# Optimization experiments

Hardware: AMD Instinct MI355X
Metric: run time of the kernel (lower is better)

Reference implementation:

```python
import math
import jax, jax.numpy as jnp
import numpy as np

B, T, D, NH = 4, 2048, 1024, 16
HS = D // NH
N_BUCKETS = 32
MAX_DIST = 128


def _relative_position_bucket(rp):
    # bidirectional T5 bucketing, n_buckets=32, max_distance=128
    nb = N_BUCKETS // 2  # 16
    buckets = (rp > 0).astype(jnp.int32) * nb
    rp = jnp.abs(rp)
    max_exact = nb // 2  # 8
    is_small = rp < max_exact
    me = max_exact - 1   # 7
    nbm = nb - 1         # 15
    rp_safe = jnp.maximum(rp, 1).astype(jnp.float32)
    rp_large = me + (jnp.log(rp_safe / me) / math.log(MAX_DIST / me) * (nbm - me)).astype(jnp.int32)
    rp_large = jnp.minimum(rp_large, nbm)
    buckets = buckets + jnp.where(is_small, rp, rp_large)
    return buckets


def compute_bias(rel_emb, qT, kT):
    ctx = jnp.arange(qT, dtype=jnp.int32)[:, None]
    mem = jnp.arange(kT, dtype=jnp.int32)[None, :]
    bucket = _relative_position_bucket(mem - ctx)  # [qT, kT]
    values = rel_emb[bucket]                        # [qT, kT, NH]
    return jnp.transpose(values, (2, 0, 1))[None]   # [1, NH, qT, kT]


def setup_inputs() -> dict:
    key = jax.random.key(0)
    ks = jax.random.split(key, 6)
    s = 0.02
    return {
        "queries": jax.random.normal(ks[0], (B, T, D), jnp.float32),
        "Wq": jax.random.normal(ks[1], (D, D), jnp.float32) * s,
        "Wk": jax.random.normal(ks[2], (D, D), jnp.float32) * s,
        "Wv": jax.random.normal(ks[3], (D, D), jnp.float32) * s,
        "Wo": jax.random.normal(ks[4], (D, D), jnp.float32) * s,
        "rel_emb": jax.random.normal(ks[5], (N_BUCKETS, NH), jnp.float32) * s,
    }


def reference(queries, Wq, Wk, Wv, Wo, rel_emb):
    b, t, d = queries.shape
    def split_heads(x):
        return jnp.transpose(x.reshape(b, t, NH, HS), (0, 2, 1, 3))  # [B, nh, T, hs]
    q = split_heads(queries @ Wq.T)
    k = split_heads(queries @ Wk.T)
    v = split_heads(queries @ Wv.T)
    att = jnp.einsum('bhqd,bhkd->bhqk', q, k) * (1.0 / math.sqrt(HS))
    att = att + compute_bias(rel_emb, t, t)
    att = jax.nn.softmax(att, axis=-1)
    o = jnp.einsum('bhqk,bhkd->bhqd', att, v)
    o = jnp.transpose(o, (0, 2, 1, 3)).reshape(b, t, d)
    return o @ Wo.T
```

## Files before the change

### kernel.cpp

```cpp
#include <hip/hip_runtime.h>
#include <math.h>

#define T_SEQ 2048
#define D_MODEL 1024
#define NHEADS 16
#define HSZ 64
#define BATCH 4

typedef __bf16 bf16x8 __attribute__((ext_vector_type(8)));
typedef __bf16 bf16x4 __attribute__((ext_vector_type(4)));
typedef short short4v __attribute__((ext_vector_type(4)));
typedef float f32x4 __attribute__((ext_vector_type(4)));
typedef float f32x16 __attribute__((ext_vector_type(16)));

__device__ __forceinline__ unsigned short f2bf(float f) {
    unsigned int u = __builtin_bit_cast(unsigned int, f);
    u += 0x7fff + ((u >> 16) & 1);
    return (unsigned short)(u >> 16);
}

__device__ __forceinline__ unsigned int pk2bf(float a, float b) {
#if __has_builtin(__builtin_amdgcn_cvt_pk_bf16_f32)
    typedef __bf16 bf16x2_t __attribute__((ext_vector_type(2)));
    bf16x2_t v = __builtin_amdgcn_cvt_pk_bf16_f32(a, b);
    return __builtin_bit_cast(unsigned int, v);
#else
    return (unsigned int)f2bf(a) | ((unsigned int)f2bf(b) << 16);
#endif
}

__device__ __forceinline__ float fexp2(float x) {
#if __has_builtin(__builtin_amdgcn_exp2f)
    return __builtin_amdgcn_exp2f(x);
#else
    return __builtin_exp2f(x);
#endif
}

__device__ __forceinline__ void pl32swap(unsigned int& a, unsigned int& b) {
#if __has_builtin(__builtin_amdgcn_permlane32_swap)
    auto r = __builtin_amdgcn_permlane32_swap((int)a, (int)b, false, false);
    a = (unsigned int)r[0];
    b = (unsigned int)r[1];
#else
    unsigned int sa = (unsigned int)__shfl_xor((int)a, 32);
    unsigned int sb = (unsigned int)__shfl_xor((int)b, 32);
    const int hi = (int)((threadIdx.x & 63) >> 5);
    unsigned int na = hi ? sb : a;
    unsigned int nb = hi ? b : sa;
    a = na; b = nb;
#endif
}

__device__ __forceinline__ void gld_lds16(const void* g, void* lds) {
    __builtin_amdgcn_global_load_lds(
        (const __attribute__((address_space(1))) unsigned int*)g,
        (__attribute__((address_space(3))) unsigned int*)lds, 16, 0, 0);
}

__device__ __forceinline__ bf16x8 ld8(const unsigned short* p) {
    return *(const bf16x8*)p;
}

__device__ __forceinline__ float t5_bias(int delta, int h, const float* __restrict__ rel) {
    int bucket = delta > 0 ? 16 : 0;
    int arp = delta < 0 ? -delta : delta;
    if (arp < 8) {
        bucket += arp;
    } else {
        float f = logf((float)arp / 7.0f) * (8.0f / logf(128.0f / 7.0f));
        int rl = 7 + (int)f;
        bucket += rl < 15 ? rl : 15;
    }
    return rel[bucket * NHEADS + h] * 1.4426950408889634f;
}

__global__ void prep(const float* __restrict__ x,
                     const float* __restrict__ w0, const float* __restrict__ w1,
                     const float* __restrict__ w2, const float* __restrict__ w3,
                     unsigned short* __restrict__ Xbf,
                     unsigned short* __restrict__ Wbf) {
    int bid = blockIdx.x;
    int tid = threadIdx.x;
    if (bid < 8192) {
        int i = bid * 256 + tid;
        float4 v = ((const float4*)x)[i];
        ushort4 o;
        o.x = f2bf(v.x); o.y = f2bf(v.y); o.z = f2bf(v.z); o.w = f2bf(v.w);
        ((ushort4*)Xbf)[i] = o;
    } else {
        int wsel = (bid - 8192) >> 10;
        const float* srcs[4] = {w0, w1, w2, w3};
        int i = ((bid - 8192) & 1023) * 256 + tid;
        float4 v = ((const float4*)srcs[wsel])[i];
        ushort4 o;
        o.x = f2bf(v.x); o.y = f2bf(v.y); o.z = f2bf(v.z); o.w = f2bf(v.w);
        ((ushort4*)(Wbf + (size_t)wsel * 1048576))[i] = o;
    }
}

template<int MODE>
__global__ __launch_bounds__(256, 2) void gemm_bt(
    const unsigned short* __restrict__ A,
    const unsigned short* __restrict__ Bw,
    void* __restrict__ out)
{
    constexpr int K = 1024;
    __shared__ __align__(16) char smem[65536];

    const int tid  = threadIdx.x;
    const int wave = tid >> 6;
    const int lane = tid & 63;
    const int quad = lane >> 4;
    const int l16  = lane & 15;
    const int wm   = wave >> 1;
    const int wn   = wave & 1;

    constexpr int NWGX = (MODE == 4) ? 24 : 8;
    const int orig = blockIdx.x + blockIdx.y * NWGX;
    constexpr int CPX = (NWGX * 64) / 8;
    const int swz  = (orig & 7) * CPX + (orig >> 3);
    const int bn   = swz % NWGX;
    const int bm   = swz / NWGX;

    const int r_in = lane >> 3;
    const int lc   = (lane & 7) ^ r_in;

    f32x4 acc[4][4];
    #pragma unroll
    for (int m = 0; m < 4; ++m)
        #pragma unroll
        for (int n = 0; n < 4; ++n)
            acc[m][n] = f32x4{0.f, 0.f, 0.f, 0.f};

    const long a_row0 = (long)bm * 128;
    const long b_row0 = (long)bn * 128;

    {
        const int k0 = lc * 8;
        unsigned short* As_ = (unsigned short*)smem;
        unsigned short* Bs_ = (unsigned short*)(smem + 16384);
        #pragma unroll
        for (int c = 0; c < 4; ++c) {
            int cc = wave * 4 + c;
            int r  = cc * 8 + r_in;
            gld_lds16(A  + (a_row0 + r) * K + k0, &As_[cc * 512]);
            gld_lds16(Bw + (b_row0 + r) * K + k0, &Bs_[cc * 512]);
        }
    }

    for (int kt = 0; kt < K / 64; ++kt) {
        const int cur = kt & 1;
        __syncthreads();

        if (kt + 1 < K / 64) {
            const int k0 = (kt + 1) * 64 + lc * 8;
            unsigned short* As_ = (unsigned short*)(smem + (cur ^ 1) * 32768);
            unsigned short* Bs_ = (unsigned short*)(smem + (cur ^ 1) * 32768 + 16384);
            #pragma unroll
            for (int c = 0; c < 4; ++c) {
                int cc = wave * 4 + c;
                int r  = cc * 8 + r_in;
                gld_lds16(A  + (a_row0 + r) * K + k0, &As_[cc * 512]);
                gld_lds16(Bw + (b_row0 + r) * K + k0, &Bs_[cc * 512]);
            }
        }

        unsigned short* As = (unsigned short*)(smem + cur * 32768);
        unsigned short* Bs = (unsigned short*)(smem + cur * 32768 + 16384);

        bf16x8 af[4][2], bf[4][2];
        #pragma unroll
        for (int m = 0; m < 4; ++m)
            #pragma unroll
            for (int ks = 0; ks < 2; ++ks) {
                int r  = wm * 64 + m * 16 + l16;
                int pc = (ks * 4 + quad) ^ (r & 7);
                af[m][ks] = ld8(&As[r * 64 + pc * 8]);
            }
        #pragma unroll
        for (int n = 0; n < 4; ++n)
            #pragma unroll
            for (int ks = 0; ks < 2; ++ks) {
                int r  = wn * 64 + n * 16 + l16;
                int pc = (ks * 4 + quad) ^ (r & 7);
                bf[n][ks] = ld8(&Bs[r * 64 + pc * 8]);
            }
        #pragma unroll
        for (int ks = 0; ks < 2; ++ks)
            #pragma unroll
            for (int m = 0; m < 4; ++m)
                #pragma unroll
                for (int n = 0; n < 4; ++n)
                    acc[m][n] = __builtin_amdgcn_mfma_f32_16x16x32_bf16(
                        af[m][ks], bf[n][ks], acc[m][n], 0, 0, 0);
    }

    const int which = (MODE == 4) ? (bn >> 3) : 0;
    if (MODE == 3) {
        float* O = (float*)out;
        #pragma unroll
        for (int m = 0; m < 4; ++m) {
            int row = bm * 128 + wm * 64 + m * 16 + quad * 4;
            #pragma unroll
            for (int n = 0; n < 4; ++n) {
                int col = bn * 128 + wn * 64 + n * 16 + l16;
                #pragma unroll
                for (int r = 0; r < 4; ++r)
                    O[(long)(row + r) * 1024 + col] = acc[m][n][r];
            }
        }
    } else if (which == 2) {
        unsigned short* O = (unsigned short*)out + (size_t)2 * 8388608;
        #pragma unroll
        for (int m = 0; m < 4; ++m) {
            int row = bm * 128 + wm * 64 + m * 16 + quad * 4;
            int b = row >> 11, t = row & 2047;
            #pragma unroll
            for (int n = 0; n < 4; ++n) {
                int cl = (bn * 128 + wn * 64 + n * 16 + l16) & 1023;
                int h = cl >> 6, hs = cl & 63;
                ushort4 pk;
                pk.x = f2bf(acc[m][n][0]); pk.y = f2bf(acc[m][n][1]);
                pk.z = f2bf(acc[m][n][2]); pk.w = f2bf(acc[m][n][3]);
                *(ushort4*)&O[(long)((b * 16 + h) * 64 + hs) * 2048 + t] = pk;
            }
        }
    } else {
        __syncthreads();
        unsigned short* Ew = (unsigned short*)smem + wave * 4608;
        const float qs = (which == 0) ? 0.125f * 1.4426950408889634f : 1.0f;
        #pragma unroll
        for (int m = 0; m < 4; ++m)
            #pragma unroll
            for (int n = 0; n < 4; ++n)
                #pragma unroll
                for (int r = 0; r < 4; ++r)
                    Ew[(m * 16 + quad * 4 + r) * 72 + n * 16 + l16] =
                        f2bf(acc[m][n][r] * qs);
        asm volatile("s_waitcnt lgkmcnt(0)" ::: "memory");

        const int cl0 = (bn * 128 + wn * 64) & 1023;
        const int h   = cl0 >> 6;
        const int gr0 = bm * 128 + wm * 64;
        const int b   = gr0 >> 11, t0 = gr0 & 2047;
        unsigned short* O = (unsigned short*)out + (size_t)which * 8388608
                          + ((size_t)(b * 16 + h) * 2048 + t0) * 64;
        #pragma unroll
        for (int rr = 0; rr < 8; ++rr) {
            int row   = rr * 8 + (lane >> 3);
            int chunk = lane & 7;
            uint4 v = *(const uint4*)&Ew[row * 72 + chunk * 8];
            *(uint4*)&O[(size_t)row * 64 + chunk * 8] = v;
        }
    }
}

__global__ __launch_bounds__(256, 4) void attn(
    const unsigned short* __restrict__ Q,
    const unsigned short* __restrict__ Kb,
    const unsigned short* __restrict__ Vt,
    const float* __restrict__ rel,
    unsigned short* __restrict__ AO)
{
    __shared__ __align__(16) char smem[33824];
    unsigned short* KsB = (unsigned short*)smem;
    unsigned short* VsB = (unsigned short*)(smem + 16384);
    float*          Bb  = (float*)(smem + 32768);

    const int tid  = threadIdx.x;
    const int wave = tid >> 6;
    const int lane = tid & 63;
    const int l31  = lane & 31;
    const int h5   = lane >> 5;

    const int bh = blockIdx.y;
    const int b  = bh >> 4, h = bh & 15;
    const int q0 = blockIdx.x * 128;

    const unsigned short* Qg = Q  + (long)bh * T_SEQ * HSZ;
    const unsigned short* Kg = Kb + (long)bh * T_SEQ * HSZ;
    const unsigned short* Vg = Vt + (long)bh * HSZ * T_SEQ;

    const int r_in = lane >> 3;
    const int lc   = (lane & 7) ^ r_in;

    {
        #pragma unroll
        for (int c = 0; c < 2; ++c) {
            int cc = wave * 2 + c;
            int r  = cc * 8 + r_in;
            gld_lds16(Kg + (long)r * 64 + lc * 8, &KsB[cc * 512]);
            gld_lds16(Vg + (long)r * T_SEQ + lc * 8, &VsB[cc * 512]);
        }
    }

    for (int i = tid; i < 263; i += 256)
        Bb[i] = t5_bias(i - 131, h, rel);

    const int qrow_lane = q0 + wave * 32 + l31;
    bf16x8 qf[4];
    #pragma unroll
    for (int hsc = 0; hsc < 4; ++hsc)
        qf[hsc] = ld8(&Qg[(long)qrow_lane * 64 + hsc * 16 + h5 * 8]);

    f32x16 o0 = {0.f,0.f,0.f,0.f,0.f,0.f,0.f,0.f,0.f,0.f,0.f,0.f,0.f,0.f,0.f,0.f};
    f32x16 o1 = o0;
    float li = 0.0f;

    const float cneg = rel[15 * NHEADS + h] * 1.4426950408889634f;
    const float cpos = rel[31 * NHEADS + h] * 1.4426950408889634f;

    for (int kt = 0; kt < T_SEQ / 64; ++kt) {
        const int cur = kt & 1;
        __syncthreads();

        if (kt + 1 < T_SEQ / 64) {
            unsigned short* Kn = KsB + (cur ^ 1) * 4096;
            unsigned short* Vn = VsB + (cur ^ 1) * 4096;
            #pragma unroll
            for (int c = 0; c < 2; ++c) {
                int cc = wave * 2 + c;
                int r  = cc * 8 + r_in;
                gld_lds16(Kg + (long)((kt + 1) * 64 + r) * 64 + lc * 8, &Kn[cc * 512]);
                gld_lds16(Vg + (long)r * T_SEQ + (kt + 1) * 64 + lc * 8, &Vn[cc * 512]);
            }
        }

        const unsigned short* Ks = KsB + cur * 4096;
        const unsigned short* Vs = VsB + cur * 4096;

        const int lo = kt * 64 - q0 - 127;
        const int hi = kt * 64 + 63 - q0;
        const bool outband = (lo >= 128) || (hi <= -128);
        const float cb = (lo >= 128) ? cpos : cneg;

        #pragma unroll
        for (int tt = 0; tt < 2; ++tt) {
            const int rk = tt * 32 + l31;
            bf16x8 af[4];
            #pragma unroll
            for (int hsc = 0; hsc < 4; ++hsc)
                af[hsc] = ld8(&Ks[rk * 64 + (((hsc << 1) | h5) ^ (rk & 7)) * 8]);

            f32x16 s;
            if (outband) {
                #pragma unroll
                for (int e = 0; e < 16; ++e) s[e] = cb;
            } else {
                const int ibase = kt * 64 + tt * 32 + h5 * 4 + 131 - qrow_lane;
                #pragma unroll
                for (int g = 0; g < 4; ++g) {
                    int i0 = ibase + g * 8;
                    i0 = i0 < 0 ? 0 : (i0 > 259 ? 259 : i0);
                    #pragma unroll
                    for (int r = 0; r < 4; ++r) s[g * 4 + r] = Bb[i0 + r];
                }
            }

            __builtin_amdgcn_s_setprio(1);
            #pragma unroll
            for (int hsc = 0; hsc < 4; ++hsc)
                s = __builtin_amdgcn_mfma_f32_32x32x16_bf16(af[hsc], qf[hsc], s, 0, 0, 0);
            __builtin_amdgcn_s_setprio(0);

            float p[16];
            #pragma unroll
            for (int e = 0; e < 16; ++e) p[e] = fexp2(s[e]);
            {
                float t0 = (p[0]  + p[1])  + (p[2]  + p[3]);
                float t1 = (p[4]  + p[5])  + (p[6]  + p[7]);
                float t2 = (p[8]  + p[9])  + (p[10] + p[11]);
                float t3 = (p[12] + p[13]) + (p[14] + p[15]);
                li += (t0 + t1) + (t2 + t3);
            }

            unsigned int x0 = pk2bf(p[0],  p[1]),  x1 = pk2bf(p[2],  p[3]);
            unsigned int y0 = pk2bf(p[4],  p[5]),  y1 = pk2bf(p[6],  p[7]);
            unsigned int z0 = pk2bf(p[8],  p[9]),  z1 = pk2bf(p[10], p[11]);
            unsigned int u0 = pk2bf(p[12], p[13]), u1 = pk2bf(p[14], p[15]);
            pl32swap(x0, y0); pl32swap(x1, y1);
            pl32swap(z0, u0); pl32swap(z1, u1);
            uint4 pw0 = {x0, x1, y0, y1};
            uint4 pw1 = {z0, z1, u0, u1};
            bf16x8 pf[2] = {__builtin_bit_cast(bf16x8, pw0),
                            __builtin_bit_cast(bf16x8, pw1)};

            #pragma unroll
            for (int c = 0; c < 2; ++c) {
                const int tc = tt * 2 + c;
                const int rv0 = l31;
                const int rv1 = 32 + l31;
                bf16x8 vf0 = ld8(&Vs[rv0 * 64 + (((tc << 1) | h5) ^ (rv0 & 7)) * 8]);
                bf16x8 vf1 = ld8(&Vs[rv1 * 64 + (((tc << 1) | h5) ^ (rv1 & 7)) * 8]);
                __builtin_amdgcn_s_setprio(1);
                o0 = __builtin_amdgcn_mfma_f32_32x32x16_bf16(pf[c], vf0, o0, 0, 0, 0);
                o1 = __builtin_amdgcn_mfma_f32_32x32x16_bf16(pf[c], vf1, o1, 0, 0, 0);
                __builtin_amdgcn_s_setprio(0);
            }
        }
    }

    li += __shfl_xor(li, 32);
    const float inv = 1.0f / li;

    #pragma unroll
    for (int g = 0; g < 4; ++g) {
        #pragma unroll
        for (int r = 0; r < 4; ++r) {
            const int ql = g * 8 + h5 * 4 + r;
            const float iv = __shfl(inv, ql);
            const int qrow = q0 + wave * 32 + ql;
            unsigned short* dst =
                &AO[(long)(b * T_SEQ + qrow) * D_MODEL + h * 64 + l31];
            dst[0]  = f2bf(o0[g * 4 + r] * iv);
            dst[32] = f2bf(o1[g * 4 + r] * iv);
        }
    }
}

extern "C" void kernel_launch(void* const* d_in, const int* in_sizes, int n_in,
                              void* d_out, int out_size, void* d_ws, size_t ws_size,
                              hipStream_t stream) {
    const float* x   = (const float*)d_in[0];
    const float* wq  = (const float*)d_in[1];
    const float* wk  = (const float*)d_in[2];
    const float* wv  = (const float*)d_in[3];
    const float* wo  = (const float*)d_in[4];
    const float* rel = (const float*)d_in[5];

    char* ws = (char*)d_ws;
    unsigned short* Xbf = (unsigned short*)(ws);
    unsigned short* Wbf = (unsigned short*)(ws + (16l << 20));
    unsigned short* Qb  = (unsigned short*)(ws + (24l << 20));

    prep<<<12288, 256, 0, stream>>>(x, wq, wk, wv, wo, Xbf, Wbf);

    gemm_bt<4><<<dim3(24, 64), 256, 0, stream>>>(Xbf, Wbf, Qb);

    unsigned short* Kbf = Qb + 8388608;
    unsigned short* Vtb = Qb + 16777216;
    unsigned short* AO  = Xbf;
    attn<<<dim3(16, 64), 256, 0, stream>>>(Qb, Kbf, Vtb, rel, AO);

    gemm_bt<3><<<dim3(8, 64), 256, 0, stream>>>(AO, Wbf + 3 * 1048576, d_out);
}
```

Baseline: 272.3 us.

## Process two query tiles per attention block with 128-key tiles for K/V reuse

Each attention block now handles 256 query rows (two 128-row tiles per wave set) and streams 128-key K/V tiles, so every K/V tile loaded to LDS feeds twice as many MFMAs. This halves the grid, doubles LDS and roughly doubles per-thread accumulators, and the launch bound drops to 2 blocks per CU. The aim is to cut global/LDS K/V traffic and sync overhead per FLOP, at the cost of occupancy and fewer blocks (512) to spread over the CUs.

```diff
diff --git a/kernel.cpp b/kernel.cpp
--- a/kernel.cpp
+++ b/kernel.cpp
@@ -256,17 +256,17 @@
     }
 }
 
-__global__ __launch_bounds__(256, 4) void attn(
+__global__ __launch_bounds__(256, 2) void attn(
     const unsigned short* __restrict__ Q,
     const unsigned short* __restrict__ Kb,
     const unsigned short* __restrict__ Vt,
     const float* __restrict__ rel,
     unsigned short* __restrict__ AO)
 {
-    __shared__ __align__(16) char smem[33824];
+    __shared__ __align__(16) char smem[66592];
     unsigned short* KsB = (unsigned short*)smem;
-    unsigned short* VsB = (unsigned short*)(smem + 16384);
-    float*          Bb  = (float*)(smem + 32768);
+    unsigned short* VsB = (unsigned short*)(smem + 32768);
+    float*          Bb  = (float*)(smem + 65536);
 
     const int tid  = threadIdx.x;
     const int wave = tid >> 6;
@@ -276,7 +276,7 @@
 
     const int bh = blockIdx.y;
     const int b  = bh >> 4, h = bh & 15;
-    const int q0 = blockIdx.x * 128;
+    const int q0 = blockIdx.x * 256;
 
     const unsigned short* Qg = Q  + (long)bh * T_SEQ * HSZ;
     const unsigned short* Kg = Kb + (long)bh * T_SEQ * HSZ;
@@ -284,137 +284,165 @@
 
     const int r_in = lane >> 3;
     const int lc   = (lane & 7) ^ r_in;
+    const int vr_l = lane >> 4;
 
     {
         #pragma unroll
-        for (int c = 0; c < 2; ++c) {
-            int cc = wave * 2 + c;
-            int r  = cc * 8 + r_in;
-            gld_lds16(Kg + (long)r * 64 + lc * 8, &KsB[cc * 512]);
-            gld_lds16(Vg + (long)r * T_SEQ + lc * 8, &VsB[cc * 512]);
+        for (int c = 0; c < 4; ++c) {
+            int cc = wave * 4 + c;
+            int kr = cc * 8 + r_in;
+            gld_lds16(Kg + (long)kr * 64 + lc * 8, &KsB[cc * 512]);
+            int vr = cc * 4 + vr_l;
+            int vch = (lane & 15) ^ (vr & 7);
+            gld_lds16(Vg + (long)vr * T_SEQ + vch * 8, &VsB[cc * 512]);
         }
     }
 
     for (int i = tid; i < 263; i += 256)
         Bb[i] = t5_bias(i - 131, h, rel);
 
-    const int qrow_lane = q0 + wave * 32 + l31;
-    bf16x8 qf[4];
+    bf16x8 qf[2][4];
     #pragma unroll
-    for (int hsc = 0; hsc < 4; ++hsc)
-        qf[hsc] = ld8(&Qg[(long)qrow_lane * 64 + hsc * 16 + h5 * 8]);
-
-    f32x16 o0 = {0.f,0.f,0.f,0.f,0.f,0.f,0.f,0.f,0.f,0.f,0.f,0.f,0.f,0.f,0.f,0.f};
-    f32x16 o1 = o0;
-    float li = 0.0f;
+    for (int qt = 0; qt < 2; ++qt) {
+        const int qrow = q0 + qt * 128 + wave * 32 + l31;
+        #pragma unroll
+        for (int hsc = 0; hsc < 4; ++hsc)
+            qf[qt][hsc] = ld8(&Qg[(long)qrow * 64 + hsc * 16 + h5 * 8]);
+    }
+
+    f32x16 o[2][2];
+    float li[2] = {0.f, 0.f};
+    #pragma unroll
+    for (int qt = 0; qt < 2; ++qt)
+        #pragma unroll
+        for (int hst = 0; hst < 2; ++hst)
+            o[qt][hst] = f32x16{0.f,0.f,0.f,0.f,0.f,0.f,0.f,0.f,
+                                0.f,0.f,0.f,0.f,0.f,0.f,0.f,0.f};
 
     const float cneg = rel[15 * NHEADS + h] * 1.4426950408889634f;
     const float cpos = rel[31 * NHEADS + h] * 1.4426950408889634f;
 
-    for (int kt = 0; kt < T_SEQ / 64; ++kt) {
+    for (int kt = 0; kt < T_SEQ / 128; ++kt) {
         const int cur = kt & 1;
         __syncthreads();
 
-        if (kt + 1 < T_SEQ / 64) {
-            unsigned short* Kn = KsB + (cur ^ 1) * 4096;
-            unsigned short* Vn = VsB + (cur ^ 1) * 4096;
-            #pragma unroll
-            for (int c = 0; c < 2; ++c) {
-                int cc = wave * 2 + c;
-                int r  = cc * 8 + r_in;
-                gld_lds16(Kg + (long)((kt + 1) * 64 + r) * 64 + lc * 8, &Kn[cc * 512]);
-                gld_lds16(Vg + (long)r * T_SEQ + (kt + 1) * 64 + lc * 8, &Vn[cc * 512]);
-            }
-        }
-
-        const unsigned short* Ks = KsB + cur * 4096;
-        const unsigned short* Vs = VsB + cur * 4096;
-
-        const int lo = kt * 64 - q0 - 127;
-        const int hi = kt * 64 + 63 - q0;
-        const bool outband = (lo >= 128) || (hi <= -128);
-        const float cb = (lo >= 128) ? cpos : cneg;
-
-        #pragma unroll
-        for (int tt = 0; tt < 2; ++tt) {
+        if (kt + 1 < T_SEQ / 128) {
+            unsigned short* Kn = KsB + (cur ^ 1) * 8192;
+            unsigned short* Vn = VsB + (cur ^ 1) * 8192;
+            #pragma unroll
+            for (int c = 0; c < 4; ++c) {
+                int cc = wave * 4 + c;
+                int kr = cc * 8 + r_in;
+                gld_lds16(Kg + (long)((kt + 1) * 128 + kr) * 64 + lc * 8, &Kn[cc * 512]);
+                int vr = cc * 4 + vr_l;
+                int vch = (lane & 15) ^ (vr & 7);
+                gld_lds16(Vg + (long)vr * T_SEQ + (kt + 1) * 128 + vch * 8, &Vn[cc * 512]);
+            }
+        }
+
+        const unsigned short* Ks = KsB + cur * 8192;
+        const unsigned short* Vs = VsB + cur * 8192;
+
+        #pragma unroll
+        for (int tt = 0; tt < 4; ++tt) {
+            const int tok_lo = kt * 128 + tt * 32;
+
             const int rk = tt * 32 + l31;
             bf16x8 af[4];
             #pragma unroll
             for (int hsc = 0; hsc < 4; ++hsc)
                 af[hsc] = ld8(&Ks[rk * 64 + (((hsc << 1) | h5) ^ (rk & 7)) * 8]);
 
-            f32x16 s;
-            if (outband) {
-                #pragma unroll
-                for (int e = 0; e < 16; ++e) s[e] = cb;
-            } else {
-                const int ibase = kt * 64 + tt * 32 + h5 * 4 + 131 - qrow_lane;
-                #pragma unroll
-                for (int g = 0; g < 4; ++g) {
-                    int i0 = ibase + g * 8;
-                    i0 = i0 < 0 ? 0 : (i0 > 259 ? 259 : i0);
+            bf16x8 pf[2][2];
+            #pragma unroll
+            for (int qt = 0; qt < 2; ++qt) {
+                const int qlo = q0 + qt * 128 + wave * 32;
+                const int dmin = tok_lo - qlo - 31;
+                const int dmax = tok_lo + 31 - qlo;
+                f32x16 s;
+                if (dmin >= 128 || dmax <= -128) {
+                    const float cb = (dmin >= 128) ? cpos : cneg;
                     #pragma unroll
-                    for (int r = 0; r < 4; ++r) s[g * 4 + r] = Bb[i0 + r];
+                    for (int e = 0; e < 16; ++e) s[e] = cb;
+                } else {
+                    const int ibase = tok_lo + h5 * 4 + 131 - (qlo + l31);
+                    #pragma unroll
+                    for (int g = 0; g < 4; ++g) {
+                        int i0 = ibase + g * 8;
+                        i0 = i0 < 0 ? 0 : (i0 > 259 ? 259 : i0);
+                        #pragma unroll
+                        for (int r = 0; r < 4; ++r) s[g * 4 + r] = Bb[i0 + r];
+                    }
                 }
-            }
-
-            __builtin_amdgcn_s_setprio(1);
-            #pragma unroll
-            for (int hsc = 0; hsc < 4; ++hsc)
-                s = __builtin_amdgcn_mfma_f32_32x32x16_bf16(af[hsc], qf[hsc], s, 0, 0, 0);
-            __builtin_amdgcn_s_setprio(0);
-
-            float p[16];
-            #pragma unroll
-            for (int e = 0; e < 16; ++e) p[e] = fexp2(s[e]);
-            {
-                float t0 = (p[0]  + p[1])  + (p[2]  + p[3]);
-                float t1 = (p[4]  + p[5])  + (p[6]  + p[7]);
-                float t2 = (p[8]  + p[9])  + (p[10] + p[11]);
-                float t3 = (p[12] + p[13]) + (p[14] + p[15]);
-                li += (t0 + t1) + (t2 + t3);
-            }
-
-            unsigned int x0 = pk2bf(p[0],  p[1]),  x1 = pk2bf(p[2],  p[3]);
-            unsigned int y0 = pk2bf(p[4],  p[5]),  y1 = pk2bf(p[6],  p[7]);
-            unsigned int z0 = pk2bf(p[8],  p[9]),  z1 = pk2bf(p[10], p[11]);
-            unsigned int u0 = pk2bf(p[12], p[13]), u1 = pk2bf(p[14], p[15]);
-            pl32swap(x0, y0); pl32swap(x1, y1);
-            pl32swap(z0, u0); pl32swap(z1, u1);
-            uint4 pw0 = {x0, x1, y0, y1};
-            uint4 pw1 = {z0, z1, u0, u1};
-            bf16x8 pf[2] = {__builtin_bit_cast(bf16x8, pw0),
-                            __builtin_bit_cast(bf16x8, pw1)};
+
+                __builtin_amdgcn_s_setprio(1);
+                #pragma unroll
+                for (int hsc = 0; hsc < 4; ++hsc)
+                    s = __builtin_amdgcn_mfma_f32_32x32x16_bf16(af[hsc], qf[qt][hsc],
+                                                                s, 0, 0, 0);
+                __builtin_amdgcn_s_setprio(0);
+
+                float p[16];
+                #pragma unroll
+                for (int e = 0; e < 16; ++e) p[e] = fexp2(s[e]);
+                {
+                    float t0 = (p[0]  + p[1])  + (p[2]  + p[3]);
+                    float t1 = (p[4]  + p[5])  + (p[6]  + p[7]);
+                    float t2 = (p[8]  + p[9])  + (p[10] + p[11]);
+                    float t3 = (p[12] + p[13]) + (p[14] + p[15]);
+                    li[qt] += (t0 + t1) + (t2 + t3);
+                }
+
+                unsigned int x0 = pk2bf(p[0],  p[1]),  x1 = pk2bf(p[2],  p[3]);
+                unsigned int y0 = pk2bf(p[4],  p[5]),  y1 = pk2bf(p[6],  p[7]);
+                unsigned int z0 = pk2bf(p[8],  p[9]),  z1 = pk2bf(p[10], p[11]);
+                unsigned int u0 = pk2bf(p[12], p[13]), u1 = pk2bf(p[14], p[15]);
+                pl32swap(x0, y0); pl32swap(x1, y1);
+                pl32swap(z0, u0); pl32swap(z1, u1);
+                uint4 pw0 = {x0, x1, y0, y1};
+                uint4 pw1 = {z0, z1, u0, u1};
+                pf[qt][0] = __builtin_bit_cast(bf16x8, pw0);
+                pf[qt][1] = __builtin_bit_cast(bf16x8, pw1);
+            }
 
             #pragma unroll
             for (int c = 0; c < 2; ++c) {
-                const int tc = tt * 2 + c;
-                const int rv0 = l31;
-                const int rv1 = 32 + l31;
-                bf16x8 vf0 = ld8(&Vs[rv0 * 64 + (((tc << 1) | h5) ^ (rv0 & 7)) * 8]);
-                bf16x8 vf1 = ld8(&Vs[rv1 * 64 + (((tc << 1) | h5) ^ (rv1 & 7)) * 8]);
+                const int ts = tt * 2 + c;
+                bf16x8 vf[2];
+                #pragma unroll
+                for (int hst = 0; hst < 2; ++hst) {
+                    const int rv = hst * 32 + l31;
+                    vf[hst] = ld8(&Vs[rv * 128 + ((ts * 2 + h5) ^ (rv & 7)) * 8]);
+                }
                 __builtin_amdgcn_s_setprio(1);
-                o0 = __builtin_amdgcn_mfma_f32_32x32x16_bf16(pf[c], vf0, o0, 0, 0, 0);
-                o1 = __builtin_amdgcn_mfma_f32_32x32x16_bf16(pf[c], vf1, o1, 0, 0, 0);
+                #pragma unroll
+                for (int qt = 0; qt < 2; ++qt) {
+                    o[qt][0] = __builtin_amdgcn_mfma_f32_32x32x16_bf16(
+                        pf[qt][c], vf[0], o[qt][0], 0, 0, 0);
+                    o[qt][1] = __builtin_amdgcn_mfma_f32_32x32x16_bf16(
+                        pf[qt][c], vf[1], o[qt][1], 0, 0, 0);
+                }
                 __builtin_amdgcn_s_setprio(0);
             }
         }
     }
 
-    li += __shfl_xor(li, 32);
-    const float inv = 1.0f / li;
-
     #pragma unroll
-    for (int g = 0; g < 4; ++g) {
-        #pragma unroll
-        for (int r = 0; r < 4; ++r) {
-            const int ql = g * 8 + h5 * 4 + r;
-            const float iv = __shfl(inv, ql);
-            const int qrow = q0 + wave * 32 + ql;
-            unsigned short* dst =
-                &AO[(long)(b * T_SEQ + qrow) * D_MODEL + h * 64 + l31];
-            dst[0]  = f2bf(o0[g * 4 + r] * iv);
-            dst[32] = f2bf(o1[g * 4 + r] * iv);
+    for (int qt = 0; qt < 2; ++qt) {
+        float lq = li[qt] + __shfl_xor(li[qt], 32);
+        const float inv = 1.0f / lq;
+        #pragma unroll
+        for (int g = 0; g < 4; ++g) {
+            #pragma unroll
+            for (int r = 0; r < 4; ++r) {
+                const int ql = g * 8 + h5 * 4 + r;
+                const float iv = __shfl(inv, ql);
+                const int qrow = q0 + qt * 128 + wave * 32 + ql;
+                unsigned short* dst =
+                    &AO[(long)(b * T_SEQ + qrow) * D_MODEL + h * 64 + l31];
+                dst[0]  = f2bf(o[qt][0][g * 4 + r] * iv);
+                dst[32] = f2bf(o[qt][1][g * 4 + r] * iv);
+            }
         }
     }
 }
@@ -441,7 +469,7 @@
     unsigned short* Kbf = Qb + 8388608;
     unsigned short* Vtb = Qb + 16777216;
     unsigned short* AO  = Xbf;
-    attn<<<dim3(16, 64), 256, 0, stream>>>(Qb, Kbf, Vtb, rel, AO);
+    attn<<<dim3(8, 64), 256, 0, stream>>>(Qb, Kbf, Vtb, rel, AO);
 
     gemm_bt<3><<<dim3(8, 64), 256, 0, stream>>>(AO, Wbf + 3 * 1048576, d_out);
 }
```

After: 353.1 us. 1.3x slower.
